# Kernel optimization log

Hardware: AMD Instinct MI355X
Metric: run time of the kernel (lower is better)

## Reference

```python
import jax, jax.numpy as jnp
import numpy as np

N = 8192      # points
NOBJ = 8      # objects
H = 64        # hidden_size (required by channel arithmetic, see notes)
CDIM = 128
K = 20
KNN = 360
EPS = 1e-5


def _lrelu(x):
    return jnp.where(x >= 0, x, 0.2 * x)


def _inorm2d(x):  # x: [C, N, K]; InstanceNorm2d, affine=False, biased var
    m = x.mean(axis=(1, 2), keepdims=True)
    v = ((x - m) ** 2).mean(axis=(1, 2), keepdims=True)
    return (x - m) / jnp.sqrt(v + EPS)


def _inorm1d(x):  # x: [C, L]
    m = x.mean(axis=1, keepdims=True)
    v = ((x - m) ** 2).mean(axis=1, keepdims=True)
    return (x - m) / jnp.sqrt(v + EPS)


def _block2d(W, f):  # 1x1 conv (no bias) + InstanceNorm2d + LeakyReLU(0.2)
    return _lrelu(_inorm2d(jnp.einsum('oc,cnk->onk', W, f)))


def _block1d(W, f):
    return _lrelu(_inorm1d(W @ f))


def _edge_feat(xc, idx):  # xc: [C, N], idx: [N, k] -> [2C, N, k]
    xt = xc.T                                   # [N, C]
    nb = xt[idx]                                # [N, k, C] gather
    ctr = jnp.broadcast_to(xt[:, None, :], nb.shape)
    return jnp.concatenate([nb - ctr, ctr], axis=2).transpose(2, 0, 1)


def _knn_idx(x, tag, k):  # kNN within same node_tag, self excluded
    xs = jax.lax.stop_gradient(x)
    sq = jnp.sum(xs * xs, axis=1)
    d2 = sq[:, None] + sq[None, :] - 2.0 * (xs @ xs.T)
    valid = (tag[:, None] == tag[None, :]) & ~jnp.eye(xs.shape[0], dtype=bool)
    d2 = jnp.where(valid, d2, jnp.inf)
    _, idx = jax.lax.top_k(-d2, k)              # ascending distance order
    return idx


def setup_inputs() -> dict:
    key = jax.random.key(0)
    ks = jax.random.split(key, 16)
    x = jax.random.normal(ks[0], (N, 3), dtype=jnp.float32)
    node_tag = (jnp.arange(N, dtype=jnp.int32) // (N // NOBJ))  # equal groups

    def w(k, o, i):
        return jax.random.normal(k, (o, i), dtype=jnp.float32) * (1.0 / np.sqrt(i))

    return {
        'x': x, 'node_tag': node_tag, 'n_obj': NOBJ,
        'W1': w(ks[1], H, 6),       'W2': w(ks[2], H, H),
        'W3': w(ks[3], H, 2 * H),   'W4': w(ks[4], H, H),
        'W5': w(ks[5], H, 2 * H),   'W6': w(ks[6], H, H),
        'W7': w(ks[7], H, 2 * H),   'W8': w(ks[8], H, H),
        'W9': w(ks[9], 128, 4 * H),
        'W10': w(ks[10], 2 * H, 3 * H),
        'W11': w(ks[11], 2 * H, 3 * H),
        'W12': w(ks[12], H, 3 * H),
        'W13': w(ks[13], H, 2 * H),
        'Wr': w(ks[14], CDIM, H),
    }


def reference(x, node_tag, n_obj, W1, W2, W3, W4, W5, W6, W7, W8, W9, W10,
              W11, W12, W13, Wr):
    n = x.shape[0]
    idx = _knn_idx(x, node_tag, KNN)            # [N, 360]

    f = _edge_feat(x.T, idx[:, :K])             # [6, N, 20]
    x1 = _block2d(W2, _block2d(W1, f)).max(axis=-1)            # [H, N]
    f = _edge_feat(x1, idx[:, :40:2])
    x2 = _block2d(W4, _block2d(W3, f)).max(axis=-1) + x1
    f = _edge_feat(x2, idx[:, :120:6])
    x3 = _block2d(W6, _block2d(W5, f)).max(axis=-1) + x2
    f = _edge_feat(x3, idx[:, :360:18])
    x4 = _block2d(W8, _block2d(W7, f)).max(axis=-1) + x3

    g = _block1d(W9, jnp.concatenate([x1, x2, x3, x4], axis=0))  # [128, N]
    g = jnp.broadcast_to(g.max(axis=1, keepdims=True), (128, n))

    x4 = _block1d(W10, jnp.concatenate([g, x4], axis=0))   # [2H, N]
    x3 = _block1d(W11, jnp.concatenate([x4, x3], axis=0))  # [2H, N]
    x2 = _block1d(W12, jnp.concatenate([x3, x2], axis=0))  # [H, N]
    x1 = _block1d(W13, jnp.concatenate([x2, x1], axis=0))  # [H, N]

    code = (Wr @ x1).T                                     # [N, c_dim]
    tag = node_tag.astype(jnp.int32)
    sums = jax.ops.segment_sum(code, tag, num_segments=n_obj)
    cnt = jax.ops.segment_sum(jnp.ones((n,), code.dtype), tag,
                              num_segments=n_obj)
    return sums / jnp.maximum(cnt, 1.0)[:, None]           # [n_obj, c_dim]
```

## Files before the change

kernel.cpp:

```cpp
#include <hip/hip_runtime.h>
#include <hip/hip_bf16.h>
#include <stdint.h>

typedef __hip_bfloat16 bf16;
typedef __attribute__((ext_vector_type(8))) short bfrag;
typedef __attribute__((ext_vector_type(4))) short s16x4;
typedef __attribute__((ext_vector_type(4))) float f32x4;

#define NPTS 8192
#define KSEL 20
#define MBIG (NPTS*KSEL)
#define EPSN 1e-5f

__device__ __forceinline__ float lrelu(float x){ return x >= 0.f ? x : 0.2f*x; }
__device__ __forceinline__ float ldx(const void* p, int i, int isbf){
  return isbf ? __bfloat162float(((const bf16*)p)[i]) : ((const float*)p)[i];
}
__device__ __forceinline__ short f2bs(float f){
  union { bf16 h; short s; } u;
  u.h = __float2bfloat16(f);
  return u.s;
}
__device__ __forceinline__ float bs2f(short s){
  return __uint_as_float(((unsigned)(unsigned short)s) << 16);
}
__device__ __forceinline__ f32x4 mfma16(bfrag a, bfrag b, f32x4 c){
  return __builtin_amdgcn_mfma_f32_16x16x32_bf16(a, b, c, 0, 0, 0);
}
__device__ __forceinline__ unsigned fenc(float x){
  unsigned u = __float_as_uint(x);
  return (u & 0x80000000u) ? ~u : (u | 0x80000000u);
}
__device__ __forceinline__ float fdec(unsigned u){
  return __uint_as_float((u & 0x80000000u) ? (u & 0x7FFFFFFFu) : ~u);
}
__device__ __forceinline__ unsigned long long u64min(unsigned long long a, unsigned long long b){ return a<b?a:b; }
__device__ __forceinline__ unsigned long long u64max(unsigned long long a, unsigned long long b){ return a<b?b:a; }
__device__ __forceinline__ void ce(unsigned long long &a, unsigned long long &b, bool asc){
  unsigned long long mn = a<b?a:b, mx = a<b?b:a;
  a = asc ? mn : mx;
  b = asc ? mx : mn;
}

__global__ void zero_kernel(float* __restrict__ p, int n){
  int i = blockIdx.x*256 + threadIdx.x;
  if (i < n) p[i] = 0.f;
}

__global__ void detect_kernel(const void* __restrict__ x, int* __restrict__ badf){
  int i = blockIdx.x*256 + threadIdx.x;
  int bad = 0;
  for (; i < NPTS*3; i += gridDim.x*256){
    float v = __bfloat162float(((const bf16*)x)[i]);
    if (!(fabsf(v) < 1000.0f)) bad = 1;
  }
  if (__any(bad) && (threadIdx.x & 63) == 0) atomicOr(badf, 1);
}

__global__ __launch_bounds__(256) void knn_kernel(const void* __restrict__ x,
                                                  const int* __restrict__ tag,
                                                  int* __restrict__ idxc,
                                                  const int* __restrict__ flagp){
  __shared__ unsigned long long keysL[1024];
  const int isbf = (*flagp == 0);
  const int i = blockIdx.x;
  const int base = (i >> 10) << 10;
  const int t = threadIdx.x;
  const float xi = ldx(x, i*3+0, isbf);
  const float yi = ldx(x, i*3+1, isbf);
  const float zi = ldx(x, i*3+2, isbf);
  const float sqi = xi*xi + yi*yi + zi*zi;
  const int tagi = tag[i];

  float cx[4], cy[4], cz[4];
  if (isbf){
    const short4* ps = (const short4*)((const bf16*)x + (size_t)(base + 4*t)*3);
    short4 a = ps[0], b = ps[1], c = ps[2];
    cx[0]=bs2f(a.x); cy[0]=bs2f(a.y); cz[0]=bs2f(a.z);
    cx[1]=bs2f(a.w); cy[1]=bs2f(b.x); cz[1]=bs2f(b.y);
    cx[2]=bs2f(b.z); cy[2]=bs2f(b.w); cz[2]=bs2f(c.x);
    cx[3]=bs2f(c.y); cy[3]=bs2f(c.z); cz[3]=bs2f(c.w);
  } else {
    const float4* pf = (const float4*)((const float*)x + (size_t)(base + 4*t)*3);
    float4 a = pf[0], b = pf[1], c = pf[2];
    cx[0]=a.x; cy[0]=a.y; cz[0]=a.z;
    cx[1]=a.w; cy[1]=b.x; cz[1]=b.y;
    cx[2]=b.z; cy[2]=b.w; cz[2]=c.x;
    cx[3]=c.y; cy[3]=c.z; cz[3]=c.w;
  }
  const int4 tg4 = *(const int4*)(tag + base + 4*t);
  const int tgs[4] = {tg4.x, tg4.y, tg4.z, tg4.w};

  unsigned long long v[4];
  #pragma unroll
  for (int r = 0; r < 4; r++){
    int gj = base + 4*t + r;
    float xj = cx[r], yj = cy[r], zj = cz[r];
    float sqj = xj*xj + yj*yj + zj*zj;
    float dot = xi*xj + yi*yj + zi*zj;
    float d2 = sqi + sqj - 2.0f*dot;
    bool valid = (gj != i) && (tgs[r] == tagi);
    unsigned k = valid ? fenc(d2) : 0xFFFFFFFFu;
    v[r] = ((unsigned long long)k << 32) | (unsigned)gj;
  }

  #pragma unroll
  for (int ksz = 2; ksz <= 1024; ksz <<= 1){
    #pragma unroll
    for (int jj = ksz >> 1; jj > 0; jj >>= 1){
      if (jj >= 256){
        __syncthreads();
        keysL[4*t+0] = v[0]; keysL[4*t+1] = v[1];
        keysL[4*t+2] = v[2]; keysL[4*t+3] = v[3];
        __syncthreads();
        const int pt = t ^ (jj >> 2);
        const bool keep_min = (((t & (ksz >> 2)) == 0) == ((t & (jj >> 2)) == 0));
        #pragma unroll
        for (int r = 0; r < 4; r++){
          unsigned long long o = keysL[4*pt + r];
          v[r] = keep_min ? u64min(v[r], o) : u64max(v[r], o);
        }
      } else if (jj >= 4){
        const int mask = jj >> 2;
        const bool keep_min = (((t & (ksz >> 2)) == 0) == ((t & mask) == 0));
        #pragma unroll
        for (int r = 0; r < 4; r++){
          unsigned long long o = __shfl_xor(v[r], mask, 64);
          v[r] = keep_min ? u64min(v[r], o) : u64max(v[r], o);
        }
      } else if (jj == 2){
        const bool asc = ((t & (ksz >> 2)) == 0);
        ce(v[0], v[2], asc);
        ce(v[1], v[3], asc);
      } else {
        if (ksz == 2){
          ce(v[0], v[1], true);
          ce(v[2], v[3], false);
        } else {
          const bool asc = ((t & (ksz >> 2)) == 0);
          ce(v[0], v[1], asc);
          ce(v[2], v[3], asc);
        }
      }
    }
  }

  __syncthreads();
  keysL[4*t+0] = v[0]; keysL[4*t+1] = v[1];
  keysL[4*t+2] = v[2]; keysL[4*t+3] = v[3];
  __syncthreads();
  if (t < 80){
    int s = t / 20, k = t - s*20;
    int step = (s == 0) ? 1 : (s == 1) ? 2 : (s == 2) ? 6 : 18;
    idxc[i*80 + t] = (int)(keysL[k*step] & 0xFFFFFFFFu);
  }
}

__global__ __launch_bounds__(256) void pq3_kernel(
    const void* __restrict__ xin, const void* __restrict__ Wc,
    float* __restrict__ Pt, float* __restrict__ Qt,
    const int* __restrict__ flagp)
{
  __shared__ float WaS[16][3], WdS[16][3];
  const int isbf = (*flagp == 0);
  const int t = threadIdx.x;
  const int n0 = (blockIdx.x & 31) * 256;
  const int cg = (blockIdx.x >> 5) * 16;
  if (t < 48){
    int r = t / 3, k = t - r*3;
    float wa = ldx(Wc, (cg + r)*6 + k, isbf);
    float wb = ldx(Wc, (cg + r)*6 + 3 + k, isbf);
    WaS[r][k] = wa; WdS[r][k] = wb - wa;
  }
  __syncthreads();
  const int n = n0 + t;
  float xr[3];
  #pragma unroll
  for (int k = 0; k < 3; k++) xr[k] = ldx(xin, n*3 + k, isbf);
  float pv[16], qv[16];
  #pragma unroll
  for (int r = 0; r < 16; r++){
    float p = 0.f, q = 0.f;
    #pragma unroll
    for (int k = 0; k < 3; k++){
      p += WaS[r][k] * xr[k];
      q += WdS[r][k] * xr[k];
    }
    pv[r] = p; qv[r] = q;
  }
  #pragma unroll
  for (int r4 = 0; r4 < 4; r4++){
    *(float4*)&Pt[n*64 + cg + r4*4] = make_float4(pv[r4*4], pv[r4*4+1], pv[r4*4+2], pv[r4*4+3]);
    *(float4*)&Qt[n*64 + cg + r4*4] = make_float4(qv[r4*4], qv[r4*4+1], qv[r4*4+2], qv[r4*4+3]);
  }
}

__global__ __launch_bounds__(256) void pqm_kernel(
    const float* __restrict__ rmaxp,
    const void* __restrict__ Wc,
    const float* __restrict__ straw,
    const float* __restrict__ resid,
    float* __restrict__ Pt, float* __restrict__ Qt,
    float* __restrict__ xout,
    const int* __restrict__ flagp)
{
  __shared__ __align__(16) short Fs[32][72];
  __shared__ float nm[64], niv[64];
  const int isbf = (*flagp == 0);
  const int t = threadIdx.x;
  const int n0 = blockIdx.x * 32;
  const int lane = t & 63, w = t >> 6;
  const int nn = lane & 15, quad = lane >> 4;

  if (t < 64){
    const float invMB = 1.0f/(float)MBIG;
    float m = straw[t] * invMB;
    float vv = straw[256+t]*invMB - m*m;
    nm[t] = m;
    niv[t] = 1.0f / sqrtf(fmaxf(vv, 0.f) + EPSN);
  }

  bfrag ap0, ap1, aq0, aq1;
  {
    const int row = 16*w + nn;
    #pragma unroll
    for (int j = 0; j < 8; j++){
      float wa0 = ldx(Wc, row*128 +      quad*8 + j, isbf);
      float wa1 = ldx(Wc, row*128 + 32 + quad*8 + j, isbf);
      float wb0 = ldx(Wc, row*128 + 64 + quad*8 + j, isbf);
      float wb1 = ldx(Wc, row*128 + 96 + quad*8 + j, isbf);
      ap0[j] = f2bs(wa0); ap1[j] = f2bs(wa1);
      aq0[j] = f2bs(wb0 - wa0); aq1[j] = f2bs(wb1 - wa1);
    }
  }
  __syncthreads();

  {
    const int jc = t & 31, kg = t >> 5;
    const int n = n0 + jc;
    #pragma unroll
    for (int u = 0; u < 2; u++){
      s16x4 pk;
      #pragma unroll
      for (int z = 0; z < 4; z++){
        int k = kg*8 + u*4 + z;
        float rv = rmaxp[k*NPTS + n];
        float vx = lrelu((rv - nm[k]) * niv[k]) + (resid ? resid[k*NPTS + n] : 0.f);
        xout[k*NPTS + n] = vx;
        pk[z] = f2bs(vx);
      }
      *(s16x4*)&Fs[jc][kg*8 + u*4] = pk;
    }
  }
  __syncthreads();

  #pragma unroll
  for (int q = 0; q < 2; q++){
    bfrag b0 = *(bfrag*)&Fs[q*16 + nn][quad*8];
    bfrag b1 = *(bfrag*)&Fs[q*16 + nn][32 + quad*8];
    f32x4 accp = {0.f,0.f,0.f,0.f}, accq = {0.f,0.f,0.f,0.f};
    accp = mfma16(ap0, b0, accp); accp = mfma16(ap1, b1, accp);
    accq = mfma16(aq0, b0, accq); accq = mfma16(aq1, b1, accq);
    int n = n0 + q*16 + nn;
    int c0 = 16*w + quad*4;
    *(float4*)&Pt[n*64 + c0] = make_float4(accp[0], accp[1], accp[2], accp[3]);
    *(float4*)&Qt[n*64 + c0] = make_float4(accq[0], accq[1], accq[2], accq[3]);
  }
}

__global__ __launch_bounds__(256) void stats1_kernel(
    const float* __restrict__ Pt, const float* __restrict__ Qt,
    const int* __restrict__ idxc, int sidx, float* __restrict__ stats)
{
  __shared__ __align__(16) float Qs[1024];
  __shared__ int ids[320];
  const int t = threadIdx.x;
  const int n0 = blockIdx.x * 16;
  for (int l = t; l < 1024; l += 256) Qs[l] = Qt[n0*64 + l];
  for (int l = t; l < 320; l += 256){
    int p = l / 20, k = l - p*20;
    ids[l] = idxc[(n0+p)*80 + sidx*20 + k] & (NPTS-1);
  }
  __syncthreads();
  const int tx = t & 15, ty = t >> 4;
  const int kq = tx >> 2, p0 = (tx & 3)*4;
  float sacc[4] = {0,0,0,0}, qacc[4] = {0,0,0,0};
  #pragma unroll
  for (int s = 0; s < 5; s++){
    int k = s*4 + kq;
    #pragma unroll
    for (int j = 0; j < 4; j++){
      int p = p0 + j;
      int nb = ids[p*20 + k];
      float4 pvv = *(const float4*)&Pt[nb*64 + ty*4];
      float4 qvv = *(const float4*)&Qs[p*64 + ty*4];
      float e0 = pvv.x+qvv.x, e1 = pvv.y+qvv.y, e2 = pvv.z+qvv.z, e3 = pvv.w+qvv.w;
      sacc[0]+=e0; sacc[1]+=e1; sacc[2]+=e2; sacc[3]+=e3;
      qacc[0]+=e0*e0; qacc[1]+=e1*e1; qacc[2]+=e2*e2; qacc[3]+=e3*e3;
    }
  }
  #pragma unroll
  for (int i = 0; i < 4; i++){
    float s = sacc[i], q = qacc[i];
    #pragma unroll
    for (int off = 8; off; off >>= 1){
      s += __shfl_down(s, off, 16);
      q += __shfl_down(q, off, 16);
    }
    if (tx == 0){
      atomicAdd(&stats[ty*4+i], s);
      atomicAdd(&stats[256+ty*4+i], q);
    }
  }
}

__global__ __launch_bounds__(256) void conv2_kernel(
    const float* __restrict__ Pt, const float* __restrict__ Qt,
    const int* __restrict__ idxc, int sidx,
    const void* __restrict__ W2c,
    const float* __restrict__ st1raw,
    float* __restrict__ stats2,
    float* __restrict__ rawmax,
    const int* __restrict__ flagp)
{
  __shared__ __align__(16) short Gs[64][72];
  __shared__ __align__(16) float Qs[1024];
  __shared__ int ids[320];
  __shared__ float nm1[64], niv1[64];
  const int isbf = (*flagp == 0);
  const int t = threadIdx.x;
  const int n0 = blockIdx.x * 16;
  const float invMB = 1.0f/(float)MBIG;

  for (int l = t; l < 1024; l += 256) Qs[l] = Qt[n0*64 + l];
  for (int l = t; l < 320; l += 256){
    int p = l / 20, k = l - p*20;
    ids[l] = idxc[(n0+p)*80 + sidx*20 + k] & (NPTS-1);
  }
  if (t < 64){
    float m = st1raw[t] * invMB;
    float v = st1raw[256+t]*invMB - m*m;
    nm1[t] = m;
    niv1[t] = 1.0f / sqrtf(fmaxf(v, 0.f) + EPSN);
  }

  const int lane = t & 63, w = t >> 6;
  const int nn = lane & 15, quad = lane >> 4;
  bfrag af0, af1;
  #pragma unroll
  for (int j = 0; j < 8; j++){
    af0[j] = f2bs(ldx(W2c, (16*w + nn)*64 +      quad*8 + j, isbf));
    af1[j] = f2bs(ldx(W2c, (16*w + nn)*64 + 32 + quad*8 + j, isbf));
  }
  __syncthreads();

  const int tx = t & 15, ty = t >> 4;
  float sacc[4] = {0,0,0,0}, qacc[4] = {0,0,0,0};
  float mxr[4] = {-3.4e38f,-3.4e38f,-3.4e38f,-3.4e38f};

  for (int s = 0; s < 5; s++){
    #pragma unroll
    for (int j = 0; j < 4; j++){
      int cg = tx*4 + j;
      int q = cg >> 4, p = cg & 15;
      int nb = ids[p*20 + s*4 + q];
      float4 pvv = *(const float4*)&Pt[nb*64 + ty*4];
      float4 qvv = *(const float4*)&Qs[p*64 + ty*4];
      s16x4 gv;
      gv[0] = f2bs(lrelu((pvv.x+qvv.x - nm1[ty*4+0]) * niv1[ty*4+0]));
      gv[1] = f2bs(lrelu((pvv.y+qvv.y - nm1[ty*4+1]) * niv1[ty*4+1]));
      gv[2] = f2bs(lrelu((pvv.z+qvv.z - nm1[ty*4+2]) * niv1[ty*4+2]));
      gv[3] = f2bs(lrelu((pvv.w+qvv.w - nm1[ty*4+3]) * niv1[ty*4+3]));
      *(s16x4*)&Gs[cg][ty*4] = gv;
    }
    __syncthreads();
    #pragma unroll
    for (int q = 0; q < 4; q++){
      bfrag b0 = *(bfrag*)&Gs[q*16 + nn][quad*8];
      bfrag b1 = *(bfrag*)&Gs[q*16 + nn][32 + quad*8];
      f32x4 acc = {0.f, 0.f, 0.f, 0.f};
      acc = mfma16(af0, b0, acc);
      acc = mfma16(af1, b1, acc);
      #pragma unroll
      for (int r = 0; r < 4; r++){
        float v = acc[r];
        sacc[r] += v; qacc[r] += v*v;
        mxr[r] = fmaxf(mxr[r], v);
      }
    }
    __syncthreads();
  }

  #pragma unroll
  for (int r = 0; r < 4; r++){
    int rr = 16*w + quad*4 + r;
    float s = sacc[r], q2 = qacc[r];
    #pragma unroll
    for (int off = 8; off; off >>= 1){
      s  += __shfl_down(s, off, 16);
      q2 += __shfl_down(q2, off, 16);
    }
    if (nn == 0){
      atomicAdd(&stats2[rr], s);
      atomicAdd(&stats2[256+rr], q2);
    }
    rawmax[rr*NPTS + n0 + nn] = mxr[r];
  }
}

__global__ __launch_bounds__(256) void gemm9_kernel(
    const void* __restrict__ W,
    const float* __restrict__ xs,
    const float* __restrict__ rmaxp, const float* __restrict__ st2raw,
    const float* __restrict__ x3, float* __restrict__ x4,
    float* __restrict__ stats, unsigned* __restrict__ maxenc,
    const int* __restrict__ flagp)
{
  __shared__ __align__(16) short Fs[64][72];
  __shared__ float nm2[64], niv2[64];
  const int t = threadIdx.x;
  const int isbf = (*flagp == 0);
  const int colbase = (blockIdx.x & 127) * 64;
  const int rb = (blockIdx.x >> 7) * 64;
  const int lane = t & 63, w = t >> 6;
  const int nn = lane & 15, quad = lane >> 4;

  if (t < 64){
    const float invMB = 1.0f/(float)MBIG;
    float m = st2raw[t] * invMB;
    float v = st2raw[256+t]*invMB - m*m;
    nm2[t] = m;
    niv2[t] = 1.0f / sqrtf(fmaxf(v, 0.f) + EPSN);
  }

  bfrag af[8];
  const int arow = rb + 16*w + nn;
  #pragma unroll
  for (int f = 0; f < 8; f++)
    #pragma unroll
    for (int j = 0; j < 8; j++)
      af[f][j] = f2bs(ldx(W, arow*256 + f*32 + quad*8 + j, isbf));

  f32x4 acc[4] = {};
  const int jcol = t & 63, kg = t >> 6;

  for (int kc = 0; kc < 256; kc += 64){
    __syncthreads();
    #pragma unroll
    for (int u = 0; u < 4; u++){
      int kl = kg*16 + u*4;
      s16x4 pk;
      #pragma unroll
      for (int z = 0; z < 4; z++){
        int k = kc + kl + z;
        float v;
        if (k < 192){
          v = xs[k*NPTS + colbase + jcol];
        } else {
          int kk = k - 192;
          float rv = rmaxp[kk*NPTS + colbase + jcol];
          v = lrelu((rv - nm2[kk]) * niv2[kk]) + x3[kk*NPTS + colbase + jcol];
          if (rb == 0) x4[kk*NPTS + colbase + jcol] = v;
        }
        pk[z] = f2bs(v);
      }
      *(s16x4*)&Fs[jcol][kl] = pk;
    }
    __syncthreads();
    const int f0 = kc >> 5;
    #pragma unroll
    for (int q = 0; q < 4; q++){
      bfrag b0 = *(bfrag*)&Fs[q*16+nn][quad*8];
      bfrag b1 = *(bfrag*)&Fs[q*16+nn][32 + quad*8];
      acc[q] = mfma16(af[f0],   b0, acc[q]);
      acc[q] = mfma16(af[f0+1], b1, acc[q]);
    }
  }

  #pragma unroll
  for (int r = 0; r < 4; r++){
    int rr = rb + 16*w + quad*4 + r;
    float sum = 0.f, q2 = 0.f, mxv = -3.4e38f;
    #pragma unroll
    for (int q = 0; q < 4; q++){
      float v = acc[q][r];
      sum += v; q2 += v*v; mxv = fmaxf(mxv, v);
    }
    #pragma unroll
    for (int off = 8; off; off >>= 1){
      sum += __shfl_down(sum, off, 16);
      q2  += __shfl_down(q2, off, 16);
      mxv  = fmaxf(mxv, __shfl_down(mxv, off, 16));
    }
    if (nn == 0){
      atomicAdd(&stats[rr], sum);
      atomicAdd(&stats[256+rr], q2);
      atomicMax(&maxenc[rr], fenc(mxv));
    }
  }
}

__global__ __launch_bounds__(256) void gemm10_kernel(
    const void* __restrict__ W,
    const float* __restrict__ B,
    const float* __restrict__ statsG, const unsigned* __restrict__ gmaxenc,
    float* __restrict__ Y,
    float* __restrict__ stats,
    const int* __restrict__ flagp)
{
  __shared__ __align__(16) short Fs[64][72];
  __shared__ float gsh[128], c0s[64];
  const int t = threadIdx.x;
  const int isbf = (*flagp == 0);
  const int colbase = (blockIdx.x & 127) * 64;
  const int rb = (blockIdx.x >> 7) * 64;
  const int lane = t & 63, w = t >> 6;
  const int nn = lane & 15, quad = lane >> 4;
  const float invMN = 1.0f/(float)NPTS;

  if (t < 128){
    float m = statsG[t] * invMN;
    float v = statsG[256+t]*invMN - m*m;
    float iv = 1.0f / sqrtf(fmaxf(v, 0.f) + EPSN);
    gsh[t] = lrelu((fdec(gmaxenc[t]) - m) * iv);
  }
  __syncthreads();
  if (t < 64){
    float s = 0.f;
    for (int j = 0; j < 128; j++) s += ldx(W, (rb + t)*192 + j, isbf) * gsh[j];
    c0s[t] = s;
  }

  bfrag af[2];
  const int arow = rb + 16*w + nn;
  #pragma unroll
  for (int f = 0; f < 2; f++)
    #pragma unroll
    for (int j = 0; j < 8; j++)
      af[f][j] = f2bs(ldx(W, arow*192 + 128 + f*32 + quad*8 + j, isbf));

  f32x4 acc[4] = {};
  const int jcol = t & 63, kg = t >> 6;

  {
    __syncthreads();
    #pragma unroll
    for (int u = 0; u < 4; u++){
      int kl = kg*16 + u*4;
      s16x4 pk;
      #pragma unroll
      for (int z = 0; z < 4; z++){
        int k = kl + z;
        pk[z] = f2bs(B[k*NPTS + colbase + jcol]);
      }
      *(s16x4*)&Fs[jcol][kl] = pk;
    }
    __syncthreads();
    #pragma unroll
    for (int q = 0; q < 4; q++){
      bfrag b0 = *(bfrag*)&Fs[q*16+nn][quad*8];
      bfrag b1 = *(bfrag*)&Fs[q*16+nn][32 + quad*8];
      acc[q] = mfma16(af[0], b0, acc[q]);
      acc[q] = mfma16(af[1], b1, acc[q]);
    }
  }

  #pragma unroll
  for (int r = 0; r < 4; r++){
    int rl = 16*w + quad*4 + r;
    int rr = rb + rl;
    float cv = c0s[rl];
    float sum = 0.f, q2 = 0.f;
    #pragma unroll
    for (int q = 0; q < 4; q++){
      float v = acc[q][r] + cv;
      sum += v; q2 += v*v;
      Y[rr*NPTS + colbase + q*16 + nn] = v;
    }
    #pragma unroll
    for (int off = 8; off; off >>= 1){
      sum += __shfl_down(sum, off, 16);
      q2  += __shfl_down(q2, off, 16);
    }
    if (nn == 0){
      atomicAdd(&stats[rr], sum);
      atomicAdd(&stats[256+rr], q2);
    }
  }
}

template<int CTOT>
__global__ __launch_bounds__(256) void gemm1d_kernel(
    const void* __restrict__ W, int ldw, int koffW,
    const float* __restrict__ A, const float* __restrict__ Araw, float invA, int CA,
    const float* __restrict__ B,
    const float* __restrict__ cvec,
    float* __restrict__ Y,
    float* __restrict__ stats, unsigned* __restrict__ maxenc,
    const int* __restrict__ flagp)
{
  __shared__ __align__(16) short Fs[64][72];
  __shared__ float am[256], aiv[256];
  const int t = threadIdx.x;
  const int isbf = (*flagp == 0);
  const int colbase = (blockIdx.x & 127) * 64;
  const int rb = (blockIdx.x >> 7) * 64;
  const int lane = t & 63, w = t >> 6;
  const int nn = lane & 15, quad = lane >> 4;

  if (Araw && t < CA){
    float m = Araw[t]*invA;
    float v = Araw[256+t]*invA - m*m;
    am[t] = m; aiv[t] = 1.0f/sqrtf(fmaxf(v,0.f)+EPSN);
  }

  constexpr int K32 = CTOT >> 5;
  bfrag af[K32];
  const int arow = rb + 16*w + nn;
  #pragma unroll
  for (int f = 0; f < K32; f++)
    #pragma unroll
    for (int j = 0; j < 8; j++)
      af[f][j] = f2bs(ldx(W, arow*ldw + koffW + f*32 + quad*8 + j, isbf));

  f32x4 acc[4] = {};
  const int jcol = t & 63, kg = t >> 6;

  for (int kc = 0; kc < CTOT; kc += 64){
    __syncthreads();
    #pragma unroll
    for (int u = 0; u < 4; u++){
      int kl = kg*16 + u*4;
      s16x4 pk;
      #pragma unroll
      for (int z = 0; z < 4; z++){
        int k = kc + kl + z;
        float v;
        if (k < CA){
          v = A[k*NPTS + colbase + jcol];
          if (Araw) v = lrelu((v - am[k]) * aiv[k]);
        } else {
          v = B[(k-CA)*NPTS + colbase + jcol];
        }
        pk[z] = f2bs(v);
      }
      *(s16x4*)&Fs[jcol][kl] = pk;
    }
    __syncthreads();
    const int f0 = kc >> 5;
    #pragma unroll
    for (int q = 0; q < 4; q++){
      bfrag b0 = *(bfrag*)&Fs[q*16+nn][quad*8];
      bfrag b1 = *(bfrag*)&Fs[q*16+nn][32 + quad*8];
      acc[q] = mfma16(af[f0],   b0, acc[q]);
      acc[q] = mfma16(af[f0+1], b1, acc[q]);
    }
  }

  #pragma unroll
  for (int r = 0; r < 4; r++){
    int rr = rb + 16*w + quad*4 + r;
    float cv = cvec ? cvec[rr] : 0.f;
    float sum = 0.f, q2 = 0.f, mxv = -3.4e38f;
    #pragma unroll
    for (int q = 0; q < 4; q++){
      float v = acc[q][r] + cv;
      sum += v; q2 += v*v; mxv = fmaxf(mxv, v);
      if (Y) Y[rr*NPTS + colbase + q*16 + nn] = v;
    }
    #pragma unroll
    for (int off = 8; off; off >>= 1){
      sum += __shfl_down(sum, off, 16);
      q2  += __shfl_down(q2, off, 16);
      mxv  = fmaxf(mxv, __shfl_down(mxv, off, 16));
    }
    if (nn == 0){
      atomicAdd(&stats[rr], sum);
      atomicAdd(&stats[256+rr], q2);
      if (maxenc) atomicMax(&maxenc[rr], fenc(mxv));
    }
  }
}

__global__ __launch_bounds__(256) void segsum_kernel(
    const float* __restrict__ ybuf, const float* __restrict__ straw,
    const int* __restrict__ tag, float* __restrict__ seg, float* __restrict__ cnt)
{
  const float invMN = 1.0f/(float)NPTS;
  int g = blockIdx.x*256 + threadIdx.x;
  int c = g >> 13, n = g & (NPTS-1);
  float m = straw[c] * invMN;
  float vv = straw[256+c]*invMN - m*m;
  float iv = 1.0f / sqrtf(fmaxf(vv, 0.f) + EPSN);
  float v = lrelu((ybuf[c*NPTS + n] - m) * iv);
  int tg = tag[n] & 7;
  int lane = threadIdx.x & 63;
  int t0 = __shfl(tg, 0, 64);
  bool uni = __all(tg == t0);
  if (uni){
    #pragma unroll
    for (int off = 32; off; off >>= 1) v += __shfl_down(v, off, 64);
    if (lane == 0){
      atomicAdd(&seg[t0*64 + c], v);
      if (c == 0) atomicAdd(cnt + t0, 64.f);
    }
  } else {
    atomicAdd(&seg[tg*64 + c], v);
    if (c == 0) atomicAdd(cnt + tg, 1.f);
  }
}

__global__ void final_kernel(const void* __restrict__ Wr,
    const float* __restrict__ seg, const float* __restrict__ cnt,
    void* __restrict__ out, int total, const int* __restrict__ flagp)
{
  const int isbf = (*flagp == 0);
  int q = blockIdx.x*blockDim.x + threadIdx.x;
  if (q >= total) return;
  int g = q >> 7, c = q & 127;
  float s = 0.f;
  for (int j = 0; j < 64; j++) s += ldx(Wr, c*64 + j, isbf) * seg[g*64 + j];
  float r = s / fmaxf(cnt[g], 1.f);
  if (isbf) ((bf16*)out)[q] = __float2bfloat16(r);
  else      ((float*)out)[q] = r;
}

extern "C" void kernel_launch(void* const* d_in, const int* in_sizes, int n_in,
                              void* d_out, int out_size, void* d_ws, size_t ws_size,
                              hipStream_t stream)
{
  const void* x   = d_in[0];
  const int* tag  = (const int*)d_in[1];
  const void* W1  = d_in[3];
  const void* W2  = d_in[4];
  const void* W3  = d_in[5];
  const void* W4  = d_in[6];
  const void* W5  = d_in[7];
  const void* W6  = d_in[8];
  const void* W7  = d_in[9];
  const void* W8  = d_in[10];
  const void* W9  = d_in[11];
  const void* W10 = d_in[12];
  const void* W11 = d_in[13];
  const void* W12 = d_in[14];
  const void* W13 = d_in[15];
  const void* Wr  = d_in[16];

  char* ws = (char*)d_ws;
  int*      idxc = (int*)ws;
  float*    xs   = (float*)(ws + 2621440);
  float* x1 = xs;
  float* x2 = xs +  64*NPTS;
  float* x3 = xs + 128*NPTS;
  float* x4 = xs + 192*NPTS;
  float*    y0   = (float*)(ws + 11010048);
  float*    y1   = (float*)(ws + 15204352);
  float*    rmax = (float*)(ws + 19398656);
  float*    Pt   = y0;
  float*    Qt   = y0 + 64*NPTS;
  float*    st   = (float*)(ws + 21495808);
  auto L = [&](int l){ return st + l*1024; };
  int*      flag     = (int*)(st + 13312);
  unsigned* gmaxenc  = (unsigned*)(st + 13440);
  float*    c0v      = st + 13568;
  float*    seg      = st + 13824;
  float*    cnt      = seg + 512;
  (void)c0v;

  zero_kernel<<<64, 256, 0, stream>>>(st, 16384);
  detect_kernel<<<12, 256, 0, stream>>>(x, flag);
  knn_kernel<<<NPTS, 256, 0, stream>>>(x, tag, idxc, flag);

  pq3_kernel<<<128, 256, 0, stream>>>(x, W1, Pt, Qt, flag);
  stats1_kernel<<<512, 256, 0, stream>>>(Pt, Qt, idxc, 0, L(0));
  conv2_kernel<<<512, 256, 0, stream>>>(Pt, Qt, idxc, 0, W2, L(0), L(1), rmax, flag);
  pqm_kernel<<<256, 256, 0, stream>>>(rmax, W3, L(1), nullptr, Pt, Qt, x1, flag);
  stats1_kernel<<<512, 256, 0, stream>>>(Pt, Qt, idxc, 1, L(2));
  conv2_kernel<<<512, 256, 0, stream>>>(Pt, Qt, idxc, 1, W4, L(2), L(3), rmax, flag);
  pqm_kernel<<<256, 256, 0, stream>>>(rmax, W5, L(3), x1, Pt, Qt, x2, flag);
  stats1_kernel<<<512, 256, 0, stream>>>(Pt, Qt, idxc, 2, L(4));
  conv2_kernel<<<512, 256, 0, stream>>>(Pt, Qt, idxc, 2, W6, L(4), L(5), rmax, flag);
  pqm_kernel<<<256, 256, 0, stream>>>(rmax, W7, L(5), x2, Pt, Qt, x3, flag);
  stats1_kernel<<<512, 256, 0, stream>>>(Pt, Qt, idxc, 3, L(6));
  conv2_kernel<<<512, 256, 0, stream>>>(Pt, Qt, idxc, 3, W8, L(6), L(7), rmax, flag);

  gemm9_kernel<<<256, 256, 0, stream>>>(W9, xs, rmax, L(7), x3, x4,
                                        L(8), gmaxenc, flag);

  const float invMN = 1.0f/(float)NPTS;
  gemm10_kernel<<<256, 256, 0, stream>>>(W10, x4, L(8), gmaxenc, y0, L(9), flag);
  gemm1d_kernel<192><<<256, 256, 0, stream>>>(W11, 192, 0, y0, L(9), invMN, 128,
                                              x3, nullptr, y1, L(10), nullptr, flag);
  gemm1d_kernel<192><<<128, 256, 0, stream>>>(W12, 192, 0, y1, L(10), invMN, 128,
                                              x2, nullptr, y0, L(11), nullptr, flag);
  gemm1d_kernel<128><<<128, 256, 0, stream>>>(W13, 128, 0, y0, L(11), invMN, 64,
                                              x1, nullptr, y1, L(12), nullptr, flag);

  segsum_kernel<<<64*NPTS/256, 256, 0, stream>>>(y1, L(12), tag, seg, cnt);
  final_kernel<<<4, 256, 0, stream>>>(Wr, seg, cnt, d_out, out_size, flag);
}
```

Measured before the change: 869.6 us.

## Sort kNN candidates per wavefront instead of per block

The kNN bitonic sort of 1024 candidates now runs in a single 64-lane wavefront holding 16 keys per lane, so each 256-thread block handles four query points. This removes the block-wide shared-memory exchange stages and their __syncthreads barriers, using register compare-exchange and cross-lane shuffles instead. The cost is more registers per thread (16 u64 keys plus coordinates), which may lower occupancy or cause spills. The output index layout is adjusted to the new lane-major ordering.

```diff
diff --git a/kernel.cpp b/kernel.cpp
--- a/kernel.cpp
+++ b/kernel.cpp
@@ -61,40 +61,54 @@
                                                   const int* __restrict__ tag,
                                                   int* __restrict__ idxc,
                                                   const int* __restrict__ flagp){
-  __shared__ unsigned long long keysL[1024];
+  __shared__ unsigned idxsh[4][1024];
   const int isbf = (*flagp == 0);
-  const int i = blockIdx.x;
+  const int t = threadIdx.x;
+  const int w = t >> 6, lane = t & 63;
+  const int i = blockIdx.x*4 + w;
   const int base = (i >> 10) << 10;
-  const int t = threadIdx.x;
   const float xi = ldx(x, i*3+0, isbf);
   const float yi = ldx(x, i*3+1, isbf);
   const float zi = ldx(x, i*3+2, isbf);
   const float sqi = xi*xi + yi*yi + zi*zi;
   const int tagi = tag[i];
 
-  float cx[4], cy[4], cz[4];
+  const int j0 = base + 16*lane;
+  float cx[16], cy[16], cz[16];
   if (isbf){
-    const short4* ps = (const short4*)((const bf16*)x + (size_t)(base + 4*t)*3);
-    short4 a = ps[0], b = ps[1], c = ps[2];
-    cx[0]=bs2f(a.x); cy[0]=bs2f(a.y); cz[0]=bs2f(a.z);
-    cx[1]=bs2f(a.w); cy[1]=bs2f(b.x); cz[1]=bs2f(b.y);
-    cx[2]=bs2f(b.z); cy[2]=bs2f(b.w); cz[2]=bs2f(c.x);
-    cx[3]=bs2f(c.y); cy[3]=bs2f(c.z); cz[3]=bs2f(c.w);
+    short sbuf[48];
+    const short4* ps = (const short4*)((const bf16*)x + (size_t)j0*3);
+    #pragma unroll
+    for (int u = 0; u < 12; u++) *(short4*)&sbuf[u*4] = ps[u];
+    #pragma unroll
+    for (int r = 0; r < 16; r++){
+      cx[r] = bs2f(sbuf[3*r+0]);
+      cy[r] = bs2f(sbuf[3*r+1]);
+      cz[r] = bs2f(sbuf[3*r+2]);
+    }
   } else {
-    const float4* pf = (const float4*)((const float*)x + (size_t)(base + 4*t)*3);
-    float4 a = pf[0], b = pf[1], c = pf[2];
-    cx[0]=a.x; cy[0]=a.y; cz[0]=a.z;
-    cx[1]=a.w; cy[1]=b.x; cz[1]=b.y;
-    cx[2]=b.z; cy[2]=b.w; cz[2]=c.x;
-    cx[3]=c.y; cy[3]=c.z; cz[3]=c.w;
-  }
-  const int4 tg4 = *(const int4*)(tag + base + 4*t);
-  const int tgs[4] = {tg4.x, tg4.y, tg4.z, tg4.w};
-
-  unsigned long long v[4];
-  #pragma unroll
-  for (int r = 0; r < 4; r++){
-    int gj = base + 4*t + r;
+    float fbuf[48];
+    const float4* pf = (const float4*)((const float*)x + (size_t)j0*3);
+    #pragma unroll
+    for (int u = 0; u < 12; u++) *(float4*)&fbuf[u*4] = pf[u];
+    #pragma unroll
+    for (int r = 0; r < 16; r++){
+      cx[r] = fbuf[3*r+0];
+      cy[r] = fbuf[3*r+1];
+      cz[r] = fbuf[3*r+2];
+    }
+  }
+  int tgs[16];
+  #pragma unroll
+  for (int u = 0; u < 4; u++){
+    int4 t4 = *(const int4*)(tag + j0 + u*4);
+    tgs[u*4+0] = t4.x; tgs[u*4+1] = t4.y; tgs[u*4+2] = t4.z; tgs[u*4+3] = t4.w;
+  }
+
+  unsigned long long v[16];
+  #pragma unroll
+  for (int r = 0; r < 16; r++){
+    int gj = j0 + r;
     float xj = cx[r], yj = cy[r], zj = cz[r];
     float sqj = xj*xj + yj*yj + zj*zj;
     float dot = xi*xj + yi*yj + zi*zj;
@@ -108,51 +122,38 @@
   for (int ksz = 2; ksz <= 1024; ksz <<= 1){
     #pragma unroll
     for (int jj = ksz >> 1; jj > 0; jj >>= 1){
-      if (jj >= 256){
-        __syncthreads();
-        keysL[4*t+0] = v[0]; keysL[4*t+1] = v[1];
-        keysL[4*t+2] = v[2]; keysL[4*t+3] = v[3];
-        __syncthreads();
-        const int pt = t ^ (jj >> 2);
-        const bool keep_min = (((t & (ksz >> 2)) == 0) == ((t & (jj >> 2)) == 0));
+      if (jj >= 16){
+        const int mask = jj >> 4;
+        const bool bk = ((lane & (ksz >> 4)) == 0);
+        const bool keep_min = (bk == ((lane & mask) == 0));
         #pragma unroll
-        for (int r = 0; r < 4; r++){
-          unsigned long long o = keysL[4*pt + r];
-          v[r] = keep_min ? u64min(v[r], o) : u64max(v[r], o);
-        }
-      } else if (jj >= 4){
-        const int mask = jj >> 2;
-        const bool keep_min = (((t & (ksz >> 2)) == 0) == ((t & mask) == 0));
-        #pragma unroll
-        for (int r = 0; r < 4; r++){
+        for (int r = 0; r < 16; r++){
           unsigned long long o = __shfl_xor(v[r], mask, 64);
           v[r] = keep_min ? u64min(v[r], o) : u64max(v[r], o);
         }
-      } else if (jj == 2){
-        const bool asc = ((t & (ksz >> 2)) == 0);
-        ce(v[0], v[2], asc);
-        ce(v[1], v[3], asc);
       } else {
-        if (ksz == 2){
-          ce(v[0], v[1], true);
-          ce(v[2], v[3], false);
-        } else {
-          const bool asc = ((t & (ksz >> 2)) == 0);
-          ce(v[0], v[1], asc);
-          ce(v[2], v[3], asc);
+        const bool ascL = (ksz >= 32) ? ((lane & (ksz >> 4)) == 0)
+                        : (ksz == 16) ? ((lane & 1) == 0) : true;
+        #pragma unroll
+        for (int r = 0; r < 16; r++){
+          if ((r & jj) == 0){
+            bool asc = (ksz <= 8) ? ((r & ksz) == 0) : ascL;
+            ce(v[r], v[r | jj], asc);
+          }
         }
       }
     }
   }
 
+  #pragma unroll
+  for (int r = 0; r < 16; r++)
+    idxsh[w][(r << 6) | lane] = (unsigned)(v[r] & 0xFFFFFFFFu);
   __syncthreads();
-  keysL[4*t+0] = v[0]; keysL[4*t+1] = v[1];
-  keysL[4*t+2] = v[2]; keysL[4*t+3] = v[3];
-  __syncthreads();
-  if (t < 80){
-    int s = t / 20, k = t - s*20;
+  for (int o = lane; o < 80; o += 64){
+    int s = o / 20, k = o - s*20;
     int step = (s == 0) ? 1 : (s == 1) ? 2 : (s == 2) ? 6 : 18;
-    idxc[i*80 + t] = (int)(keysL[k*step] & 0xFFFFFFFFu);
+    int p = k*step;
+    idxc[i*80 + o] = (int)idxsh[w][((p & 15) << 6) | (p >> 4)];
   }
 }
 
@@ -762,14 +763,12 @@
   auto L = [&](int l){ return st + l*1024; };
   int*      flag     = (int*)(st + 13312);
   unsigned* gmaxenc  = (unsigned*)(st + 13440);
-  float*    c0v      = st + 13568;
   float*    seg      = st + 13824;
   float*    cnt      = seg + 512;
-  (void)c0v;
 
   zero_kernel<<<64, 256, 0, stream>>>(st, 16384);
   detect_kernel<<<12, 256, 0, stream>>>(x, flag);
-  knn_kernel<<<NPTS, 256, 0, stream>>>(x, tag, idxc, flag);
+  knn_kernel<<<2048, 256, 0, stream>>>(x, tag, idxc, flag);
 
   pq3_kernel<<<128, 256, 0, stream>>>(x, W1, Pt, Qt, flag);
   stats1_kernel<<<512, 256, 0, stream>>>(Pt, Qt, idxc, 0, L(0));
```

Result: faster. 851.8 us (median of 2 runs) (-2.0%).
